# Kernel optimization log

Measured on AMD Instinct MI355X. Metric: run time of the kernel, lower is better.

The kernel has to match this reference:

```python
import jax, jax.numpy as jnp
import numpy as np

B, S, D, R = 32, 4096, 2048, 128
LN_EPS = 1e-5


def setup_inputs() -> dict:
    key = jax.random.key(0)
    ks = jax.random.split(key, 5)
    input_embeds = jax.random.normal(ks[0], (B, S, D), dtype=jnp.float32)
    query = jax.random.normal(ks[1], (1, D), dtype=jnp.float32)
    # Linear weights stored as [in, out]; scaled like torch default init (~1/sqrt(in))
    Wq = jax.random.normal(ks[2], (D, R), dtype=jnp.float32) * (1.0 / np.sqrt(D))
    We = jax.random.normal(ks[3], (D, R), dtype=jnp.float32) * (1.0 / np.sqrt(D))
    bq = jnp.zeros((R,), dtype=jnp.float32)
    be = jnp.zeros((R,), dtype=jnp.float32)
    ln_gamma = jnp.ones((D,), dtype=jnp.float32)
    ln_beta = jnp.zeros((D,), dtype=jnp.float32)
    return {"input_embeds": input_embeds, "query": query, "Wq": Wq, "bq": bq,
            "We": We, "be": be, "ln_gamma": ln_gamma, "ln_beta": ln_beta}


def reference(input_embeds, query, Wq, bq, We, be, ln_gamma, ln_beta):
    # qq: project the single learnable query -> [R]
    qq = (query @ Wq + bq)[0]                                   # [R]
    # kk: project every token -> [B, S, R]
    kk = jnp.einsum("bsd,dr->bsr", input_embeds, We) + be       # [B, S, R]
    # scores of the single query against all tokens
    score = jnp.einsum("r,bsr->bs", qq, kk) / jnp.sqrt(jnp.float32(R))  # [B, S]
    attn = jax.nn.softmax(score, axis=-1)                       # [B, S]
    # weighted sum of the ORIGINAL embeddings (not the projected ones)
    g = jnp.einsum("bs,bsd->bd", attn, input_embeds)            # [B, D]
    # LayerNorm over last dim
    mean = jnp.mean(g, axis=-1, keepdims=True)
    var = jnp.mean(jnp.square(g - mean), axis=-1, keepdims=True)
    out = (g - mean) * jax.lax.rsqrt(var + LN_EPS) * ln_gamma + ln_beta
    return out
```

## Files before the change

### kernel.cpp

```cpp
#include <hip/hip_runtime.h>
#include <math.h>

#define D 2048
#define R 128
#define NB 32
#define NS 4096
#define PSTRIDE (D + 16)
#define PQ 2304
#define PBASE 4352
#define RSQRT_R 0.08838834764831845f
#define LN_EPS 1e-5f

typedef float f4 __attribute__((ext_vector_type(4)));

__global__ __launch_bounds__(128) void k_qq1(const float* __restrict__ query,
                                             const float* __restrict__ Wq,
                                             float* __restrict__ pq) {
    const int r = threadIdx.x, blk = blockIdx.x;
    const int d0 = blk * (D / 16);
    float acc = 0.f;
    #pragma unroll 8
    for (int d = 0; d < D / 16; ++d)
        acc = fmaf(query[d0 + d], Wq[(size_t)(d0 + d) * R + r], acc);
    pq[blk * R + r] = acc;
}

__global__ __launch_bounds__(256) void k_w(const float* __restrict__ We,
                                           const float* __restrict__ bq,
                                           const float* __restrict__ be,
                                           float* __restrict__ ws) {
    __shared__ float sqq[R], sc[R];
    const int tid = threadIdx.x;
    const float* pq = ws + PQ;
    if (tid < R) {
        float q = bq[tid];
        #pragma unroll
        for (int i = 0; i < 16; ++i) q += pq[i * R + tid];
        sqq[tid] = q;
        sc[tid] = q * be[tid];
    }
    __syncthreads();
    for (int off = 64; off > 0; off >>= 1) {
        if (tid < off) sc[tid] += sc[tid + off];
        __syncthreads();
    }
    if (blockIdx.x == 0 && tid == 0) ws[D + R] = sc[0];

    const int d = blockIdx.x * 256 + tid;
    const f4* row = reinterpret_cast<const f4*>(We + (size_t)d * R);
    float a0 = 0.f, a1 = 0.f;
    #pragma unroll
    for (int r4 = 0; r4 < R / 4; r4 += 2) {
        const f4 v0 = row[r4], v1 = row[r4 + 1];
        a0 = fmaf(v0[0], sqq[r4 * 4 + 0], a0);
        a0 = fmaf(v0[1], sqq[r4 * 4 + 1], a0);
        a0 = fmaf(v0[2], sqq[r4 * 4 + 2], a0);
        a0 = fmaf(v0[3], sqq[r4 * 4 + 3], a0);
        a1 = fmaf(v1[0], sqq[r4 * 4 + 4], a1);
        a1 = fmaf(v1[1], sqq[r4 * 4 + 5], a1);
        a1 = fmaf(v1[2], sqq[r4 * 4 + 6], a1);
        a1 = fmaf(v1[3], sqq[r4 * 4 + 7], a1);
    }
    ws[d] = a0 + a1;
}

__global__ __launch_bounds__(256) void k_main(const float* __restrict__ X,
                                              const float* __restrict__ ws,
                                              float* __restrict__ partials,
                                              int cpb, int rpc) {
    const int b = blockIdx.y, chunk = blockIdx.x;
    const int tid = threadIdx.x;
    const int lane = tid & 63, wid = tid >> 6;

    f4 w4[8];
    #pragma unroll
    for (int k = 0; k < 8; ++k)
        w4[k] = *reinterpret_cast<const f4*>(ws + lane * 4 + k * 256);
    const float c = ws[D + R];

    const int s0 = chunk * rpc;
    const int s1 = s0 + rpc;

    float m = -INFINITY, l = 0.f;
    f4 acc[8];
    #pragma unroll
    for (int k = 0; k < 8; ++k) acc[k] = (f4)(0.f);

    for (int s = s0 + wid; s < s1; s += 8) {
        const float* ra = X + ((size_t)b * NS + s) * D + lane * 4;
        const float* rb = ra + 4 * D;
        f4 xa[8], xb[8];
        #pragma unroll
        for (int k = 0; k < 8; ++k)
            xa[k] = __builtin_nontemporal_load(reinterpret_cast<const f4*>(ra + k * 256));
        #pragma unroll
        for (int k = 0; k < 8; ++k)
            xb[k] = __builtin_nontemporal_load(reinterpret_cast<const f4*>(rb + k * 256));

        float da0 = 0.f, da1 = 0.f, db0 = 0.f, db1 = 0.f;
        #pragma unroll
        for (int k = 0; k < 8; k += 2) {
            da0 = fmaf(xa[k][0], w4[k][0], da0);
            da0 = fmaf(xa[k][1], w4[k][1], da0);
            da0 = fmaf(xa[k][2], w4[k][2], da0);
            da0 = fmaf(xa[k][3], w4[k][3], da0);
            da1 = fmaf(xa[k+1][0], w4[k+1][0], da1);
            da1 = fmaf(xa[k+1][1], w4[k+1][1], da1);
            da1 = fmaf(xa[k+1][2], w4[k+1][2], da1);
            da1 = fmaf(xa[k+1][3], w4[k+1][3], da1);
            db0 = fmaf(xb[k][0], w4[k][0], db0);
            db0 = fmaf(xb[k][1], w4[k][1], db0);
            db0 = fmaf(xb[k][2], w4[k][2], db0);
            db0 = fmaf(xb[k][3], w4[k][3], db0);
            db1 = fmaf(xb[k+1][0], w4[k+1][0], db1);
            db1 = fmaf(xb[k+1][1], w4[k+1][1], db1);
            db1 = fmaf(xb[k+1][2], w4[k+1][2], db1);
            db1 = fmaf(xb[k+1][3], w4[k+1][3], db1);
        }
        float da = da0 + da1, db = db0 + db1;
        #pragma unroll
        for (int off = 32; off > 0; off >>= 1) {
            da += __shfl_xor(da, off, 64);
            db += __shfl_xor(db, off, 64);
        }
        const float sa = (da + c) * RSQRT_R;
        const float sb = (db + c) * RSQRT_R;
        const float mn = fmaxf(sa, sb);

        if (mn > m) {
            const float f = __expf(m - mn);
            l *= f;
            #pragma unroll
            for (int k = 0; k < 8; ++k) acc[k] *= f;
            m = mn;
        }
        const float pa = __expf(sa - m);
        const float pb = __expf(sb - m);
        l += pa + pb;
        #pragma unroll
        for (int k = 0; k < 8; ++k) acc[k] += pa * xa[k] + pb * xb[k];
    }

    __shared__ float sm[4], sl[4];
    __shared__ __align__(16) float sacc[4][D];
    if (lane == 0) { sm[wid] = m; sl[wid] = l; }
    __syncthreads();
    const float mb = fmaxf(fmaxf(sm[0], sm[1]), fmaxf(sm[2], sm[3]));
    const float lb = __expf(sm[0] - mb) * sl[0] + __expf(sm[1] - mb) * sl[1] +
                     __expf(sm[2] - mb) * sl[2] + __expf(sm[3] - mb) * sl[3];
    const float coeff = __expf(m - mb);
    #pragma unroll
    for (int k = 0; k < 8; ++k)
        *reinterpret_cast<f4*>(&sacc[wid][lane * 4 + k * 256]) = acc[k] * coeff;
    __syncthreads();

    float* rec = partials + (size_t)(b * cpb + chunk) * PSTRIDE;
    {
        const int i0 = tid * 4, i1 = 1024 + tid * 4;
        f4 r0 = *reinterpret_cast<const f4*>(&sacc[0][i0]) +
                *reinterpret_cast<const f4*>(&sacc[1][i0]) +
                *reinterpret_cast<const f4*>(&sacc[2][i0]) +
                *reinterpret_cast<const f4*>(&sacc[3][i0]);
        f4 r1 = *reinterpret_cast<const f4*>(&sacc[0][i1]) +
                *reinterpret_cast<const f4*>(&sacc[1][i1]) +
                *reinterpret_cast<const f4*>(&sacc[2][i1]) +
                *reinterpret_cast<const f4*>(&sacc[3][i1]);
        *reinterpret_cast<f4*>(rec + i0) = r0;
        *reinterpret_cast<f4*>(rec + i1) = r1;
    }
    if (tid == 0) { rec[D] = mb; rec[D + 1] = lb; }
}

__global__ __launch_bounds__(512) void k_fin(const float* __restrict__ partials,
                                             const float* __restrict__ gamma,
                                             const float* __restrict__ beta,
                                             float* __restrict__ out, int cpb) {
    const int b = blockIdx.x, tid = threadIdx.x;
    __shared__ float scoef[64];
    __shared__ float sredA[512], sredB[512];
    const float* pb = partials + (size_t)b * cpb * PSTRIDE;

    float mloc = -INFINITY;
    for (int i = tid; i < cpb; i += 512) mloc = fmaxf(mloc, pb[i * PSTRIDE + D]);
    sredA[tid] = mloc; __syncthreads();
    for (int off = 256; off > 0; off >>= 1) {
        if (tid < off) sredA[tid] = fmaxf(sredA[tid], sredA[tid + off]);
        __syncthreads();
    }
    const float mg = sredA[0];
    __syncthreads();

    float lloc = 0.f;
    for (int i = tid; i < cpb; i += 512) {
        const float cf = __expf(pb[i * PSTRIDE + D] - mg);
        scoef[i] = cf;
        lloc += cf * pb[i * PSTRIDE + D + 1];
    }
    sredA[tid] = lloc; __syncthreads();
    for (int off = 256; off > 0; off >>= 1) {
        if (tid < off) sredA[tid] += sredA[tid + off];
        __syncthreads();
    }
    const float inv_l = 1.f / sredA[0];
    __syncthreads();

    f4 g = (f4)(0.f);
    for (int i = 0; i < cpb; ++i) {
        const float cf = scoef[i];
        const f4 a = *reinterpret_cast<const f4*>(pb + (size_t)i * PSTRIDE + tid * 4);
        g[0] = fmaf(cf, a[0], g[0]);
        g[1] = fmaf(cf, a[1], g[1]);
        g[2] = fmaf(cf, a[2], g[2]);
        g[3] = fmaf(cf, a[3], g[3]);
    }
    g *= inv_l;

    const float s1 = g[0] + g[1] + g[2] + g[3];
    const float s2 = g[0]*g[0] + g[1]*g[1] + g[2]*g[2] + g[3]*g[3];
    sredA[tid] = s1; sredB[tid] = s2; __syncthreads();
    for (int off = 256; off > 0; off >>= 1) {
        if (tid < off) { sredA[tid] += sredA[tid + off]; sredB[tid] += sredB[tid + off]; }
        __syncthreads();
    }
    const float mean = sredA[0] / (float)D;
    const float var = sredB[0] / (float)D - mean * mean;
    const float rstd = rsqrtf(var + LN_EPS);

    const f4 ga = *reinterpret_cast<const f4*>(gamma + tid * 4);
    const f4 be = *reinterpret_cast<const f4*>(beta + tid * 4);
    f4 o;
    o[0] = (g[0] - mean) * rstd * ga[0] + be[0];
    o[1] = (g[1] - mean) * rstd * ga[1] + be[1];
    o[2] = (g[2] - mean) * rstd * ga[2] + be[2];
    o[3] = (g[3] - mean) * rstd * ga[3] + be[3];
    *reinterpret_cast<f4*>(out + (size_t)b * D + tid * 4) = o;
}

extern "C" void kernel_launch(void* const* d_in, const int* in_sizes, int n_in,
                              void* d_out, int out_size, void* d_ws, size_t ws_size,
                              hipStream_t stream) {
    const float* X     = (const float*)d_in[0];
    const float* query = (const float*)d_in[1];
    const float* Wq    = (const float*)d_in[2];
    const float* bq    = (const float*)d_in[3];
    const float* We    = (const float*)d_in[4];
    const float* be    = (const float*)d_in[5];
    const float* gamma = (const float*)d_in[6];
    const float* beta  = (const float*)d_in[7];
    float* out = (float*)d_out;
    float* ws  = (float*)d_ws;

    size_t avail = ws_size / 4;
    int cpb = 32;
    while (cpb > 1 && (size_t)PBASE + (size_t)NB * cpb * PSTRIDE > avail) cpb >>= 1;
    const int rpc = NS / cpb;

    hipLaunchKernelGGL(k_qq1, dim3(16), dim3(128), 0, stream, query, Wq, ws + PQ);
    hipLaunchKernelGGL(k_w, dim3(D / 256), dim3(256), 0, stream, We, bq, be, ws);
    hipLaunchKernelGGL(k_main, dim3(cpb, NB), dim3(256), 0, stream,
                       X, ws, ws + PBASE, cpb, rpc);
    hipLaunchKernelGGL(k_fin, dim3(NB), dim3(512), 0, stream,
                       ws + PBASE, gamma, beta, out, cpb);
}
```

Baseline: 183.6 us.

## Fuse prologue kernels with grid barrier and finalize into main via last-block counter

Merges the two small projection kernels into one 8-block kernel that synchronises its blocks through an atomic counter spin-wait. It also folds the finalize (softmax merge plus LayerNorm) into the main kernel, where the last block per batch, found via an atomic ticket, does the reduction. This removes two kernel launches and their gaps but adds a memset launch, atomics, and a spin barrier that relies on all 8 blocks being co-resident.

```diff
diff --git a/kernel.cpp b/kernel.cpp
--- a/kernel.cpp
+++ b/kernel.cpp
@@ -6,60 +6,84 @@
 #define NB 32
 #define NS 4096
 #define PSTRIDE (D + 16)
-#define PQ 2304
-#define PBASE 4352
+#define PQOFF 2048
+#define COFF 3072
+#define CNTOFF 3076
+#define PBASE 3200
 #define RSQRT_R 0.08838834764831845f
 #define LN_EPS 1e-5f
 
 typedef float f4 __attribute__((ext_vector_type(4)));
 
-__global__ __launch_bounds__(128) void k_qq1(const float* __restrict__ query,
+__global__ __launch_bounds__(256) void k_pro(const float* __restrict__ query,
                                              const float* __restrict__ Wq,
-                                             float* __restrict__ pq) {
-    const int r = threadIdx.x, blk = blockIdx.x;
-    const int d0 = blk * (D / 16);
-    float acc = 0.f;
-    #pragma unroll 8
-    for (int d = 0; d < D / 16; ++d)
-        acc = fmaf(query[d0 + d], Wq[(size_t)(d0 + d) * R + r], acc);
-    pq[blk * R + r] = acc;
-}
-
-__global__ __launch_bounds__(256) void k_w(const float* __restrict__ We,
-                                           const float* __restrict__ bq,
-                                           const float* __restrict__ be,
-                                           float* __restrict__ ws) {
-    __shared__ float sqq[R], sc[R];
-    const int tid = threadIdx.x;
-    const float* pq = ws + PQ;
-    if (tid < R) {
-        float q = bq[tid];
-        #pragma unroll
-        for (int i = 0; i < 16; ++i) q += pq[i * R + tid];
-        sqq[tid] = q;
-        sc[tid] = q * be[tid];
-    }
-    __syncthreads();
-    for (int off = 64; off > 0; off >>= 1) {
-        if (tid < off) sc[tid] += sc[tid + off];
+                                             const float* __restrict__ bq,
+                                             const float* __restrict__ be,
+                                             const float* __restrict__ We,
+                                             float* __restrict__ ws,
+                                             int* __restrict__ cnt) {
+    __shared__ f4 sp[256];
+    __shared__ float sqq[R];
+    const int tid = threadIdx.x, blk = blockIdx.x;
+    const int r4 = tid & 31, dd = tid >> 5;
+    const f4* Wq4 = reinterpret_cast<const f4*>(Wq);
+
+    const int dg0 = blk * 256 + dd * 32;
+    f4 acc = (f4)(0.f);
+    #pragma unroll
+    for (int i = 0; i < 32; ++i)
+        acc += query[dg0 + i] * Wq4[(size_t)(dg0 + i) * 32 + r4];
+    sp[tid] = acc;
+    __syncthreads();
+    #pragma unroll
+    for (int off = 4; off > 0; off >>= 1) {
+        if (dd < off) sp[tid] += sp[tid + off * 32];
         __syncthreads();
     }
-    if (blockIdx.x == 0 && tid == 0) ws[D + R] = sc[0];
-
-    const int d = blockIdx.x * 256 + tid;
+    if (tid < 32) reinterpret_cast<f4*>(ws + PQOFF + blk * R)[tid] = sp[tid];
+    __threadfence();
+    __syncthreads();
+    if (tid == 0) {
+        atomicAdd(cnt, 1);
+        while (__hip_atomic_load(cnt, __ATOMIC_ACQUIRE, __HIP_MEMORY_SCOPE_AGENT) < 8)
+            __builtin_amdgcn_s_sleep(2);
+    }
+    __syncthreads();
+    __threadfence();
+
+    if (tid < 32) {
+        f4 q = reinterpret_cast<const f4*>(bq)[tid];
+        #pragma unroll
+        for (int i = 0; i < 8; ++i)
+            q += reinterpret_cast<const f4*>(ws + PQOFF + i * R)[tid];
+        reinterpret_cast<f4*>(sqq)[tid] = q;
+        sp[tid] = q * reinterpret_cast<const f4*>(be)[tid];
+    }
+    __syncthreads();
+    #pragma unroll
+    for (int off = 16; off > 0; off >>= 1) {
+        if (tid < off) sp[tid] += sp[tid + off];
+        __syncthreads();
+    }
+    if (blk == 0 && tid == 0) {
+        const f4 t = sp[0];
+        ws[COFF] = t[0] + t[1] + t[2] + t[3];
+    }
+
+    const int d = blk * 256 + tid;
     const f4* row = reinterpret_cast<const f4*>(We + (size_t)d * R);
     float a0 = 0.f, a1 = 0.f;
     #pragma unroll
-    for (int r4 = 0; r4 < R / 4; r4 += 2) {
-        const f4 v0 = row[r4], v1 = row[r4 + 1];
-        a0 = fmaf(v0[0], sqq[r4 * 4 + 0], a0);
-        a0 = fmaf(v0[1], sqq[r4 * 4 + 1], a0);
-        a0 = fmaf(v0[2], sqq[r4 * 4 + 2], a0);
-        a0 = fmaf(v0[3], sqq[r4 * 4 + 3], a0);
-        a1 = fmaf(v1[0], sqq[r4 * 4 + 4], a1);
-        a1 = fmaf(v1[1], sqq[r4 * 4 + 5], a1);
-        a1 = fmaf(v1[2], sqq[r4 * 4 + 6], a1);
-        a1 = fmaf(v1[3], sqq[r4 * 4 + 7], a1);
+    for (int q4 = 0; q4 < 32; q4 += 2) {
+        const f4 v0 = row[q4], v1 = row[q4 + 1];
+        a0 = fmaf(v0[0], sqq[q4 * 4 + 0], a0);
+        a0 = fmaf(v0[1], sqq[q4 * 4 + 1], a0);
+        a0 = fmaf(v0[2], sqq[q4 * 4 + 2], a0);
+        a0 = fmaf(v0[3], sqq[q4 * 4 + 3], a0);
+        a1 = fmaf(v1[0], sqq[q4 * 4 + 4], a1);
+        a1 = fmaf(v1[1], sqq[q4 * 4 + 5], a1);
+        a1 = fmaf(v1[2], sqq[q4 * 4 + 6], a1);
+        a1 = fmaf(v1[3], sqq[q4 * 4 + 7], a1);
     }
     ws[d] = a0 + a1;
 }
@@ -67,6 +91,10 @@
 __global__ __launch_bounds__(256) void k_main(const float* __restrict__ X,
                                               const float* __restrict__ ws,
                                               float* __restrict__ partials,
+                                              int* __restrict__ cntb,
+                                              const float* __restrict__ gamma,
+                                              const float* __restrict__ beta,
+                                              float* __restrict__ out,
                                               int cpb, int rpc) {
     const int b = blockIdx.y, chunk = blockIdx.x;
     const int tid = threadIdx.x;
@@ -76,7 +104,7 @@
     #pragma unroll
     for (int k = 0; k < 8; ++k)
         w4[k] = *reinterpret_cast<const f4*>(ws + lane * 4 + k * 256);
-    const float c = ws[D + R];
+    const float c = ws[COFF];
 
     const int s0 = chunk * rpc;
     const int s1 = s0 + rpc;
@@ -169,71 +197,70 @@
         *reinterpret_cast<f4*>(rec + i1) = r1;
     }
     if (tid == 0) { rec[D] = mb; rec[D + 1] = lb; }
-}
-
-__global__ __launch_bounds__(512) void k_fin(const float* __restrict__ partials,
-                                             const float* __restrict__ gamma,
-                                             const float* __restrict__ beta,
-                                             float* __restrict__ out, int cpb) {
-    const int b = blockIdx.x, tid = threadIdx.x;
-    __shared__ float scoef[64];
-    __shared__ float sredA[512], sredB[512];
-    const float* pb = partials + (size_t)b * cpb * PSTRIDE;
-
-    float mloc = -INFINITY;
-    for (int i = tid; i < cpb; i += 512) mloc = fmaxf(mloc, pb[i * PSTRIDE + D]);
-    sredA[tid] = mloc; __syncthreads();
-    for (int off = 256; off > 0; off >>= 1) {
-        if (tid < off) sredA[tid] = fmaxf(sredA[tid], sredA[tid + off]);
+
+    __threadfence();
+    __syncthreads();
+    __shared__ int slast;
+    if (tid == 0) {
+        const int old = atomicAdd(cntb + b, 1);
+        slast = (old == cpb - 1);
+    }
+    __syncthreads();
+    if (!slast) return;
+    __threadfence();
+
+    const float* pbase = partials + (size_t)b * cpb * PSTRIDE;
+    __shared__ float smm[32], sll[32];
+    if (tid < cpb) {
+        smm[tid] = pbase[(size_t)tid * PSTRIDE + D];
+        sll[tid] = pbase[(size_t)tid * PSTRIDE + D + 1];
+    }
+    __syncthreads();
+    float mg = -INFINITY;
+    for (int i = 0; i < cpb; ++i) mg = fmaxf(mg, smm[i]);
+    float lg = 0.f;
+    for (int i = 0; i < cpb; ++i) lg += __expf(smm[i] - mg) * sll[i];
+    const float inv_l = 1.f / lg;
+
+    f4 g0 = (f4)(0.f), g1 = (f4)(0.f);
+    for (int i = 0; i < cpb; ++i) {
+        const float cf = __expf(smm[i] - mg);
+        const f4 a0 = *reinterpret_cast<const f4*>(pbase + (size_t)i * PSTRIDE + tid * 4);
+        const f4 a1 = *reinterpret_cast<const f4*>(pbase + (size_t)i * PSTRIDE + 1024 + tid * 4);
+        g0 += cf * a0;
+        g1 += cf * a1;
+    }
+    g0 *= inv_l; g1 *= inv_l;
+
+    const float s1v = g0[0]+g0[1]+g0[2]+g0[3]+g1[0]+g1[1]+g1[2]+g1[3];
+    const float s2v = g0[0]*g0[0]+g0[1]*g0[1]+g0[2]*g0[2]+g0[3]*g0[3]+
+                      g1[0]*g1[0]+g1[1]*g1[1]+g1[2]*g1[2]+g1[3]*g1[3];
+    __shared__ float sA[256], sB[256];
+    sA[tid] = s1v; sB[tid] = s2v;
+    __syncthreads();
+    for (int off = 128; off > 0; off >>= 1) {
+        if (tid < off) { sA[tid] += sA[tid + off]; sB[tid] += sB[tid + off]; }
         __syncthreads();
     }
-    const float mg = sredA[0];
-    __syncthreads();
-
-    float lloc = 0.f;
-    for (int i = tid; i < cpb; i += 512) {
-        const float cf = __expf(pb[i * PSTRIDE + D] - mg);
-        scoef[i] = cf;
-        lloc += cf * pb[i * PSTRIDE + D + 1];
-    }
-    sredA[tid] = lloc; __syncthreads();
-    for (int off = 256; off > 0; off >>= 1) {
-        if (tid < off) sredA[tid] += sredA[tid + off];
-        __syncthreads();
-    }
-    const float inv_l = 1.f / sredA[0];
-    __syncthreads();
-
-    f4 g = (f4)(0.f);
-    for (int i = 0; i < cpb; ++i) {
-        const float cf = scoef[i];
-        const f4 a = *reinterpret_cast<const f4*>(pb + (size_t)i * PSTRIDE + tid * 4);
-        g[0] = fmaf(cf, a[0], g[0]);
-        g[1] = fmaf(cf, a[1], g[1]);
-        g[2] = fmaf(cf, a[2], g[2]);
-        g[3] = fmaf(cf, a[3], g[3]);
-    }
-    g *= inv_l;
-
-    const float s1 = g[0] + g[1] + g[2] + g[3];
-    const float s2 = g[0]*g[0] + g[1]*g[1] + g[2]*g[2] + g[3]*g[3];
-    sredA[tid] = s1; sredB[tid] = s2; __syncthreads();
-    for (int off = 256; off > 0; off >>= 1) {
-        if (tid < off) { sredA[tid] += sredA[tid + off]; sredB[tid] += sredB[tid + off]; }
-        __syncthreads();
-    }
-    const float mean = sredA[0] / (float)D;
-    const float var = sredB[0] / (float)D - mean * mean;
+    const float mean = sA[0] / (float)D;
+    const float var  = sB[0] / (float)D - mean * mean;
     const float rstd = rsqrtf(var + LN_EPS);
 
-    const f4 ga = *reinterpret_cast<const f4*>(gamma + tid * 4);
-    const f4 be = *reinterpret_cast<const f4*>(beta + tid * 4);
-    f4 o;
-    o[0] = (g[0] - mean) * rstd * ga[0] + be[0];
-    o[1] = (g[1] - mean) * rstd * ga[1] + be[1];
-    o[2] = (g[2] - mean) * rstd * ga[2] + be[2];
-    o[3] = (g[3] - mean) * rstd * ga[3] + be[3];
-    *reinterpret_cast<f4*>(out + (size_t)b * D + tid * 4) = o;
+    const f4 ga0 = *reinterpret_cast<const f4*>(gamma + tid * 4);
+    const f4 ga1 = *reinterpret_cast<const f4*>(gamma + 1024 + tid * 4);
+    const f4 be0 = *reinterpret_cast<const f4*>(beta + tid * 4);
+    const f4 be1 = *reinterpret_cast<const f4*>(beta + 1024 + tid * 4);
+    f4 o0, o1;
+    o0[0] = (g0[0] - mean) * rstd * ga0[0] + be0[0];
+    o0[1] = (g0[1] - mean) * rstd * ga0[1] + be0[1];
+    o0[2] = (g0[2] - mean) * rstd * ga0[2] + be0[2];
+    o0[3] = (g0[3] - mean) * rstd * ga0[3] + be0[3];
+    o1[0] = (g1[0] - mean) * rstd * ga1[0] + be1[0];
+    o1[1] = (g1[1] - mean) * rstd * ga1[1] + be1[1];
+    o1[2] = (g1[2] - mean) * rstd * ga1[2] + be1[2];
+    o1[3] = (g1[3] - mean) * rstd * ga1[3] + be1[3];
+    *reinterpret_cast<f4*>(out + (size_t)b * D + tid * 4) = o0;
+    *reinterpret_cast<f4*>(out + (size_t)b * D + 1024 + tid * 4) = o1;
 }
 
 extern "C" void kernel_launch(void* const* d_in, const int* in_sizes, int n_in,
@@ -249,16 +276,16 @@
     const float* beta  = (const float*)d_in[7];
     float* out = (float*)d_out;
     float* ws  = (float*)d_ws;
+    int*   cnt = (int*)((char*)d_ws + (size_t)CNTOFF * 4);
 
     size_t avail = ws_size / 4;
     int cpb = 32;
     while (cpb > 1 && (size_t)PBASE + (size_t)NB * cpb * PSTRIDE > avail) cpb >>= 1;
     const int rpc = NS / cpb;
 
-    hipLaunchKernelGGL(k_qq1, dim3(16), dim3(128), 0, stream, query, Wq, ws + PQ);
-    hipLaunchKernelGGL(k_w, dim3(D / 256), dim3(256), 0, stream, We, bq, be, ws);
+    hipMemsetAsync((void*)cnt, 0, 33 * sizeof(int), stream);
+    hipLaunchKernelGGL(k_pro, dim3(8), dim3(256), 0, stream,
+                       query, Wq, bq, be, We, ws, cnt);
     hipLaunchKernelGGL(k_main, dim3(cpb, NB), dim3(256), 0, stream,
-                       X, ws, ws + PBASE, cpb, rpc);
-    hipLaunchKernelGGL(k_fin, dim3(NB), dim3(512), 0, stream,
-                       ws + PBASE, gamma, beta, out, cpb);
+                       X, ws, ws + PBASE, cnt + 1, gamma, beta, out, cpb, rpc);
 }
```

New measurement: 430.7 us. +134.6%, slower.
